# Kernel tuning notes

Hardware: AMD Instinct MI355X
Metric: run time of the kernel (lower is better)

The kernel has to match this reference:

```python
import jax, jax.numpy as jnp
import numpy as np

ROTARY_DIM = 128
ROTARY_BASE = 10000.0
ATTN_SCALE = 11.313708498984761  # sqrt(d_head=128)
N_HEADS = 16
N_KV = 4


def _apply_rotary(x, rotary_dim, rotary_base):
    # x: [seq, heads, d_head]
    seq_len = x.shape[0]
    dim_pairs = rotary_dim // 2
    freqs = 1.0 / rotary_base ** (jnp.arange(dim_pairs, dtype=jnp.float32) / dim_pairs)
    angles = jnp.outer(jnp.arange(seq_len), freqs)  # [seq, pairs]
    cos = jnp.cos(angles)[:, None, :]
    sin = jnp.sin(angles)[:, None, :]
    x_rot = x[..., :rotary_dim]
    x_pass = x[..., rotary_dim:]
    x1 = x_rot[..., ::2]
    x2 = x_rot[..., 1::2]
    out1 = x1 * cos - x2 * sin
    out2 = x1 * sin + x2 * cos
    rotated = jnp.stack([out1, out2], axis=-1).reshape(x_rot.shape)
    return jnp.concatenate([rotated, x_pass], axis=-1)


def setup_inputs() -> dict:
    key = jax.random.key(0)
    ks = jax.random.split(key, 5)
    seq, d_model, d_head = 4096, 2048, 128
    scale = 1.0 / np.sqrt(d_model)
    return {
        "x": jax.random.normal(ks[0], (seq, d_model), jnp.float32),
        "W_Q": jax.random.normal(ks[1], (N_HEADS, d_model, d_head), jnp.float32) * scale,
        "W_K": jax.random.normal(ks[2], (N_KV, d_model, d_head), jnp.float32) * scale,
        "W_V": jax.random.normal(ks[3], (N_KV, d_model, d_head), jnp.float32) * scale,
        "W_O": jax.random.normal(ks[4], (N_HEADS, d_head, d_model), jnp.float32) * scale,
        "b_Q": jnp.zeros((N_HEADS, d_head), jnp.float32),
        "b_K": jnp.zeros((N_KV, d_head), jnp.float32),
        "b_V": jnp.zeros((N_KV, d_head), jnp.float32),
        "b_O": jnp.zeros((2048,), jnp.float32),
    }


def reference(x, W_Q, W_K, W_V, W_O, b_Q, b_K, b_V, b_O):
    seq_len = x.shape[0]
    q = jnp.einsum('sm,nmh->snh', x, W_Q) + b_Q  # [s, 16, 128]
    k = jnp.einsum('sm,nmh->snh', x, W_K) + b_K  # [s, 4, 128]
    v = jnp.einsum('sm,nmh->snh', x, W_V) + b_V
    q = _apply_rotary(q, ROTARY_DIM, ROTARY_BASE)
    k = _apply_rotary(k, ROTARY_DIM, ROTARY_BASE)
    repeats = N_HEADS // N_KV
    k = jnp.repeat(k, repeats, axis=1)
    v = jnp.repeat(v, repeats, axis=1)
    attn_scores = jnp.einsum('qnh,knh->nqk', q, k) / ATTN_SCALE
    mask = jnp.tril(jnp.ones((seq_len, seq_len), dtype=jnp.bool_))
    attn_scores = jnp.where(mask[None, :, :], attn_scores,
                            jnp.finfo(attn_scores.dtype).min)
    pattern = jax.nn.softmax(attn_scores, axis=-1)
    z = jnp.einsum('nqk,knh->qnh', pattern, v)
    return jnp.einsum('snh,nhm->sm', z, W_O) + b_O
```

## Files before the change

### kernel.cpp

```cpp
#include <hip/hip_runtime.h>
#include <hip/hip_bf16.h>
#include <cstdint>
#include <cstddef>

#define SEQ    4096
#define DM     2048
#define DH     128
#define NH     16
#define NKV    4
#define NC     3072
#define KOFF   2048
#define VOFF   2560
#define Q_SCALE 0.12751730f

using bf16 = __hip_bfloat16;
typedef __bf16 bf16x8 __attribute__((ext_vector_type(8)));
typedef float f32x4 __attribute__((ext_vector_type(4)));
typedef float f32x16 __attribute__((ext_vector_type(16)));

static __device__ inline float bf2f(bf16 x) { return __bfloat162float(x); }
static __device__ inline bf16 f2bf(float x) { return __float2bfloat16(x); }

static __device__ inline void load_lds16(const bf16* g, bf16* l) {
    __builtin_amdgcn_global_load_lds(
        (const __attribute__((address_space(1))) uint32_t*)g,
        (__attribute__((address_space(3))) uint32_t*)l, 16, 0, 0);
}

__global__ void xconv(const float* __restrict__ in, bf16* __restrict__ out) {
    int i = blockIdx.x * 256 + threadIdx.x;
    float4 v = ((const float4*)in)[i];
    bf16 a = f2bf(v.x), b = f2bf(v.y), c = f2bf(v.z), d = f2bf(v.w);
    ushort4 u;
    u.x = *(unsigned short*)&a; u.y = *(unsigned short*)&b;
    u.z = *(unsigned short*)&c; u.w = *(unsigned short*)&d;
    ((ushort4*)out)[i] = u;
}

__global__ void prep_wqkv(const float* __restrict__ WQ, const float* __restrict__ WK,
                          const float* __restrict__ WV, bf16* __restrict__ wt) {
    __shared__ float tl[64][65];
    const int t = threadIdx.x;
    const int m0 = (int)blockIdx.x * 64;
    const int head = (int)blockIdx.y >> 1;
    const int h0 = ((int)blockIdx.y & 1) * 64;
    const float* src = (head < 16) ? WQ + (size_t)head * DM * DH
                     : (head < 20) ? WK + (size_t)(head - 16) * DM * DH
                                   : WV + (size_t)(head - 20) * DM * DH;
    {
        const int r = t >> 2, c = (t & 3) * 16;
        const float* p = src + (size_t)(m0 + r) * DH + h0 + c;
        #pragma unroll
        for (int kk = 0; kk < 4; ++kk) {
            float4 v = *(const float4*)(p + kk * 4);
            tl[r][c + kk * 4 + 0] = v.x; tl[r][c + kk * 4 + 1] = v.y;
            tl[r][c + kk * 4 + 2] = v.z; tl[r][c + kk * 4 + 3] = v.w;
        }
    }
    __syncthreads();
    {
        const int hh = t >> 2, ms = (t & 3) * 16;
        const int j = head * 128 + h0 + hh;
        bf16 tmp[16];
        #pragma unroll
        for (int i = 0; i < 16; ++i) tmp[i] = f2bf(tl[ms + i][hh]);
        bf16* q = wt + (size_t)j * DM + m0 + ms;
        *(bf16x8*)q       = *(bf16x8*)&tmp[0];
        *(bf16x8*)(q + 8) = *(bf16x8*)&tmp[8];
    }
}

__global__ void prep_wo(const float* __restrict__ WO, bf16* __restrict__ wt) {
    __shared__ float tl[64][65];
    const int t = threadIdx.x;
    const int m0 = (int)blockIdx.x * 64;
    const int j0 = (int)blockIdx.y * 64;
    {
        const int r = t >> 2, c = (t & 3) * 16;
        const float* p = WO + (size_t)(m0 + r) * DM + j0 + c;
        #pragma unroll
        for (int kk = 0; kk < 4; ++kk) {
            float4 v = *(const float4*)(p + kk * 4);
            tl[r][c + kk * 4 + 0] = v.x; tl[r][c + kk * 4 + 1] = v.y;
            tl[r][c + kk * 4 + 2] = v.z; tl[r][c + kk * 4 + 3] = v.w;
        }
    }
    __syncthreads();
    {
        const int hh = t >> 2, ms = (t & 3) * 16;
        bf16 tmp[16];
        #pragma unroll
        for (int i = 0; i < 16; ++i) tmp[i] = f2bf(tl[ms + i][hh]);
        bf16* q = wt + (size_t)(j0 + hh) * DM + m0 + ms;
        *(bf16x8*)q       = *(bf16x8*)&tmp[0];
        *(bf16x8*)(q + 8) = *(bf16x8*)&tmp[8];
    }
}

__global__ void prep_bias(const float* __restrict__ bQ, const float* __restrict__ bK,
                          const float* __restrict__ bV, float* __restrict__ bias) {
    int j = blockIdx.x * 256 + threadIdx.x;
    if (j >= NC) return;
    bias[j] = (j < KOFF) ? bQ[j] : (j < VOFF ? bK[j - KOFF] : bV[j - VOFF]);
}

__global__ void sctab(float2* __restrict__ tab) {
    int idx = blockIdx.x * 256 + threadIdx.x;
    int s = idx >> 6, i = idx & 63;
    float inv_freq = __expf(-(float)i * 0.14391156831212788f);
    float ang = (float)s * inv_freq;
    float2 cs;
    cs.x = cosf(ang);
    cs.y = sinf(ang);
    tab[idx] = cs;
}

#define BM 128
#define BN 128
#define BK 64

template <typename OutT, int ROT>
__global__ __launch_bounds__(256)
void gemm_bt(const bf16* __restrict__ A, const bf16* __restrict__ Bt,
             const float* __restrict__ bias, OutT* __restrict__ C, int N,
             const float2* __restrict__ tab) {
    __shared__ __align__(16) bf16 As[BM * BK];
    __shared__ __align__(16) bf16 Bs[BN * BK];
    const int tid = threadIdx.x;
    const int wave = tid >> 6, lane = tid & 63;
    const int quad = lane >> 4, l15 = lane & 15;
    const int wm = (wave >> 1) * 64, wn = (wave & 1) * 64;
    const int m0 = blockIdx.y * BM, n0 = blockIdx.x * BN;

    f32x4 acc[4][4] = {};

    const bf16* gsrc = (wave < 2)
        ? A  + (size_t)(m0 + (wave & 1) * 64) * DM
        : Bt + (size_t)(n0 + (wave & 1) * 64) * DM;
    bf16* lbase = (wave < 2 ? As : Bs) + (wave & 1) * 64 * BK;
    const int lrow = lane >> 3;
    const int gslot = (lane & 7) ^ lrow;
    const bf16* gp = gsrc + (size_t)lrow * DM + gslot * 8;

    const int rsw = l15 & 7;

    for (int k0 = 0; k0 < DM; k0 += BK) {
        __syncthreads();
        #pragma unroll
        for (int cc = 0; cc < 8; ++cc)
            load_lds16(gp + (size_t)cc * 8 * DM + k0, lbase + cc * 8 * BK);
        __syncthreads();

        #pragma unroll
        for (int ks = 0; ks < 2; ++ks) {
            bf16x8 af[4], bfr[4];
            #pragma unroll
            for (int i = 0; i < 4; ++i)
                af[i] = *(const bf16x8*)&As[(wm + i * 16 + l15) * BK + (((ks * 4 + quad) ^ rsw) * 8)];
            #pragma unroll
            for (int j = 0; j < 4; ++j)
                bfr[j] = *(const bf16x8*)&Bs[(wn + j * 16 + l15) * BK + (((ks * 4 + quad) ^ rsw) * 8)];
            #pragma unroll
            for (int i = 0; i < 4; ++i)
                #pragma unroll
                for (int j = 0; j < 4; ++j)
                    acc[i][j] = __builtin_amdgcn_mfma_f32_16x16x32_bf16(af[i], bfr[j], acc[i][j], 0, 0, 0);
        }
    }

    const bool doRot = ROT && (n0 < VOFF);
    const float scl = (n0 < KOFF) ? Q_SCALE : 1.0f;

    #pragma unroll
    for (int i = 0; i < 4; ++i) {
        int row = m0 + wm + i * 16 + quad * 4;
        #pragma unroll
        for (int j = 0; j < 4; ++j) {
            int col = n0 + wn + j * 16 + l15;
            float bv = bias[col];
            if (ROT && doRot) {
                const int ii = (col >> 1) & 63;
                const bool odd = col & 1;
                #pragma unroll
                for (int r = 0; r < 4; ++r) {
                    float v = acc[i][j][r] + bv;
                    float pv = __shfl_xor(v, 1);
                    float2 cs = tab[((row + r) << 6) + ii];
                    float o = odd ? (pv * cs.y + v * cs.x) : (v * cs.x - pv * cs.y);
                    C[(size_t)(row + r) * N + col] = (OutT)f2bf(o * scl);
                }
            } else {
                #pragma unroll
                for (int r = 0; r < 4; ++r) {
                    float val = acc[i][j][r] + bv;
                    if constexpr (sizeof(OutT) == 2)
                        C[(size_t)(row + r) * N + col] = f2bf(val);
                    else
                        C[(size_t)(row + r) * N + col] = val;
                }
            }
        }
    }
}

__global__ void vtrans(const bf16* __restrict__ qkv, bf16* __restrict__ vt) {
    __shared__ bf16 tl[64][72];
    const int t = threadIdx.x;
    const int s0 = (int)(blockIdx.x >> 3) * 64;
    const int c0 = (int)(blockIdx.x & 7) * 64;
    {
        int r = t >> 2, cc = (t & 3) * 16;
        const bf16* p = qkv + (size_t)(s0 + r) * NC + VOFF + c0 + cc;
        *(bf16x8*)&tl[r][cc]     = *(const bf16x8*)p;
        *(bf16x8*)&tl[r][cc + 8] = *(const bf16x8*)(p + 8);
    }
    __syncthreads();
    {
        int dd = t >> 2, sc = (t & 3) * 16;
        int col = c0 + dd;
        bf16 tmp[16];
        #pragma unroll
        for (int j = 0; j < 16; ++j) tmp[j] = tl[sc + j][dd];
        bf16* q = vt + (size_t)col * SEQ + s0 + sc;
        *(bf16x8*)q       = *(bf16x8*)&tmp[0];
        *(bf16x8*)(q + 8) = *(bf16x8*)&tmp[8];
    }
}

__global__ __launch_bounds__(256)
void flash(const bf16* __restrict__ qkv, const bf16* __restrict__ vt,
           bf16* __restrict__ z) {
    __shared__ __align__(16) char smem[65536];
    float* ob  = (float*)smem;
    float* lml = (float*)(smem + 32768);

    const int tid = threadIdx.x;
    const int wave = tid >> 6, lane = tid & 63;
    const int l31 = lane & 31, lh = lane >> 5;
    const int ch = wave >> 1;
    const int kh = wave & 1;
    const int bx = blockIdx.x;
    const int qt = 127 - (bx >> 3);
    const int g = (bx >> 1) & 3;
    const int hp = bx & 1;
    const int r_base = qt * 32 + ch * 16;
    const int ktmax = qt >> 1;
    const int rsw = l31 & 7;

    const bf16* kp[4];
    const bf16* vp[4];
    #pragma unroll
    for (int i = 0; i < 4; ++i) {
        const int q = wave * 4 + i;
        const int krow = q * 4 + (lane >> 4);
        kp[i] = qkv + KOFF + g * DH + (size_t)krow * NC + (((lane & 15) ^ (krow & 7)) * 8);
        const int vdd = q * 8 + (lane >> 3);
        vp[i] = vt + (size_t)(g * DH + vdd) * SEQ + (((lane & 7) ^ (vdd & 7)) * 8);
    }

    {
        bf16* Ksb = (bf16*)smem;
        bf16* Vsb = (bf16*)(smem + 16384);
        #pragma unroll
        for (int i = 0; i < 4; ++i) load_lds16(kp[i], Ksb + (wave * 4 + i) * 512);
        #pragma unroll
        for (int i = 0; i < 4; ++i) load_lds16(vp[i], Vsb + (wave * 4 + i) * 512);
        #pragma unroll
        for (int i = 0; i < 4; ++i) { kp[i] += (size_t)64 * NC; vp[i] += 64; }
    }

    bf16x8 qf[8];
    {
        const int qrow = r_base + (l31 & 15);
        const int head = g * 4 + hp * 2 + (l31 >> 4);
        const bf16* qp = qkv + (size_t)qrow * NC + head * DH + lh * 8;
        #pragma unroll
        for (int s = 0; s < 8; ++s)
            qf[s] = *(const bf16x8*)(qp + s * 16);
    }

    f32x16 o_acc[4] = {};
    float lsum = 0.0f;
    int cur = 0;

    for (int kt = 0; kt <= ktmax; ++kt) {
        __syncthreads();
        if (kt < ktmax) {
            bf16* Ksb = (bf16*)(smem + (cur ^ 1) * 32768);
            bf16* Vsb = (bf16*)(smem + (cur ^ 1) * 32768 + 16384);
            #pragma unroll
            for (int i = 0; i < 4; ++i) load_lds16(kp[i], Ksb + (wave * 4 + i) * 512);
            #pragma unroll
            for (int i = 0; i < 4; ++i) load_lds16(vp[i], Vsb + (wave * 4 + i) * 512);
            #pragma unroll
            for (int i = 0; i < 4; ++i) { kp[i] += (size_t)64 * NC; vp[i] += 64; }
        }
        const bf16* Ks = (const bf16*)(smem + cur * 32768);
        const bf16* Vs = (const bf16*)(smem + cur * 32768 + 16384);
        cur ^= 1;

        const int key_min = kt * 64 + kh * 32;
        if (key_min <= r_base + 15) {
            f32x16 sa = {}, sb = {};
            __builtin_amdgcn_s_setprio(1);
            #pragma unroll
            for (int s = 0; s < 4; ++s) {
                bf16x8 kb0 = *(const bf16x8*)&Ks[(kh * 32 + l31) * 128 + (((lh + 4 * s) ^ rsw) * 8)];
                sa = __builtin_amdgcn_mfma_f32_32x32x16_bf16(kb0, qf[2 * s], sa, 0, 0, 0);
                bf16x8 kb1 = *(const bf16x8*)&Ks[(kh * 32 + l31) * 128 + (((lh + 4 * s + 2) ^ rsw) * 8)];
                sb = __builtin_amdgcn_mfma_f32_32x32x16_bf16(kb1, qf[2 * s + 1], sb, 0, 0, 0);
            }
            __builtin_amdgcn_s_setprio(0);
            f32x16 sacc = sa + sb;

            const bool needmask = (key_min + 31 > r_base);
            const int qrow = r_base + (l31 & 15);
            float e[16];
            if (needmask) {
                #pragma unroll
                for (int rg = 0; rg < 16; ++rg) {
                    const int keyg = key_min + (rg & 3) + 8 * (rg >> 2) + 4 * lh;
                    float sv = sacc[rg];
                    if (keyg > qrow) sv = -INFINITY;
                    e[rg] = exp2f(sv);
                }
            } else {
                #pragma unroll
                for (int rg = 0; rg < 16; ++rg)
                    e[rg] = exp2f(sacc[rg]);
            }
            {
                float t0 = (e[0] + e[1]) + (e[2] + e[3]);
                float t1 = (e[4] + e[5]) + (e[6] + e[7]);
                float t2 = (e[8] + e[9]) + (e[10] + e[11]);
                float t3 = (e[12] + e[13]) + (e[14] + e[15]);
                lsum += (t0 + t1) + (t2 + t3);
            }

            bf16x8 pa[2];
            #pragma unroll
            for (int s2 = 0; s2 < 2; ++s2) {
                uint32_t wA0, wA1, wB0, wB1;
                asm("v_cvt_pk_bf16_f32 %0, %1, %2" : "=v"(wA0) : "v"(e[8*s2+0]), "v"(e[8*s2+1]));
                asm("v_cvt_pk_bf16_f32 %0, %1, %2" : "=v"(wA1) : "v"(e[8*s2+2]), "v"(e[8*s2+3]));
                asm("v_cvt_pk_bf16_f32 %0, %1, %2" : "=v"(wB0) : "v"(e[8*s2+4]), "v"(e[8*s2+5]));
                asm("v_cvt_pk_bf16_f32 %0, %1, %2" : "=v"(wB1) : "v"(e[8*s2+6]), "v"(e[8*s2+7]));
                asm volatile("v_permlane32_swap_b32 %0, %1" : "+v"(wA0), "+v"(wB0));
                asm volatile("v_permlane32_swap_b32 %0, %1" : "+v"(wA1), "+v"(wB1));
                union { uint32_t u[4]; bf16x8 v; } cvt;
                cvt.u[0] = wA0; cvt.u[1] = wA1; cvt.u[2] = wB0; cvt.u[3] = wB1;
                pa[s2] = cvt.v;
            }

            __builtin_amdgcn_s_setprio(1);
            #pragma unroll
            for (int s2 = 0; s2 < 2; ++s2) {
                #pragma unroll
                for (int nt = 0; nt < 4; ++nt) {
                    bf16x8 vb = *(const bf16x8*)&Vs[(nt * 32 + l31) * 64 + (((kh * 4 + lh + 2 * s2) ^ rsw) * 8)];
                    o_acc[nt] = __builtin_amdgcn_mfma_f32_32x32x16_bf16(pa[s2], vb, o_acc[nt], 0, 0, 0);
                }
            }
            __builtin_amdgcn_s_setprio(0);
        }
    }

    float la = lsum, lb = lsum;
    asm volatile("v_permlane32_swap_b32 %0, %1" : "+v"(la), "+v"(lb));
    const float l_tot = la + lb;

    __syncthreads();
    if (lh == 0) lml[wave * 32 + l31] = l_tot;
    if (kh == 1) {
        #pragma unroll
        for (int nt = 0; nt < 4; ++nt)
            #pragma unroll
            for (int rg = 0; rg < 16; ++rg) {
                const int m = (rg & 3) + 8 * (rg >> 2) + 4 * lh;
                ob[(ch * 32 + m) * 128 + nt * 32 + l31] = o_acc[nt][rg];
            }
    }
    __syncthreads();
    if (kh == 0) {
        float invl[16];
        #pragma unroll
        for (int rg = 0; rg < 16; ++rg) {
            const int m = (rg & 3) + 8 * (rg >> 2) + 4 * lh;
            invl[rg] = 1.0f / (lml[wave * 32 + m] + lml[(wave + 1) * 32 + m]);
        }
        #pragma unroll
        for (int nt = 0; nt < 4; ++nt)
            #pragma unroll
            for (int rg = 0; rg < 16; ++rg) {
                const int m = (rg & 3) + 8 * (rg >> 2) + 4 * lh;
                float oo = o_acc[nt][rg] + ob[(ch * 32 + m) * 128 + nt * 32 + l31];
                const int row = r_base + (m & 15);
                const int col = (g * 4 + hp * 2 + (m >> 4)) * DH + nt * 32 + l31;
                z[(size_t)row * DM + col] = f2bf(oo * invl[rg]);
            }
    }
}

extern "C" void kernel_launch(void* const* d_in, const int* in_sizes, int n_in,
                              void* d_out, int out_size, void* d_ws, size_t ws_size,
                              hipStream_t stream) {
    const float* x  = (const float*)d_in[0];
    const float* WQ = (const float*)d_in[1];
    const float* WK = (const float*)d_in[2];
    const float* WV = (const float*)d_in[3];
    const float* WO = (const float*)d_in[4];
    const float* bQ = (const float*)d_in[5];
    const float* bK = (const float*)d_in[6];
    const float* bV = (const float*)d_in[7];
    const float* bO = (const float*)d_in[8];
    float* out = (float*)d_out;

    char* ws = (char*)d_ws;
    bf16*  wt_cat = (bf16*)(ws);
    bf16*  wt_o   = (bf16*)(ws + 12582912);
    float* bias_c = (float*)(ws + 20971520);
    bf16*  qkv    = (bf16*)(ws + 20987904);
    bf16*  vt     = (bf16*)(ws + 46153728);
    bf16*  z      = (bf16*)(ws + 50348032);
    bf16*  xb     = (bf16*)(ws + 67125248);
    float2* sct   = (float2*)vt;

    xconv    <<<8192, 256, 0, stream>>>(x, xb);
    prep_wqkv<<<dim3(32, 48), 256, 0, stream>>>(WQ, WK, WV, wt_cat);
    prep_wo  <<<dim3(32, 32), 256, 0, stream>>>(WO, wt_o);
    prep_bias<<<12, 256, 0, stream>>>(bQ, bK, bV, bias_c);
    sctab    <<<1024, 256, 0, stream>>>(sct);
    gemm_bt<bf16, 1> <<<dim3(24, 32), 256, 0, stream>>>(xb, wt_cat, bias_c, qkv, NC, sct);
    vtrans   <<<512, 256, 0, stream>>>(qkv, vt);
    flash    <<<1024, 256, 0, stream>>>(qkv, vt, z);
    gemm_bt<float, 0><<<dim3(16, 32), 256, 0, stream>>>(z, wt_o, bO, out, DM, nullptr);
}
```

Before: 376.5 us.

## Replace double-buffered K/V LDS pipeline with single buffer and serial MFMA chains

```diff
diff --git a/kernel.cpp b/kernel.cpp
--- a/kernel.cpp
+++ b/kernel.cpp
@@ -230,9 +230,11 @@
 __global__ __launch_bounds__(256)
 void flash(const bf16* __restrict__ qkv, const bf16* __restrict__ vt,
            bf16* __restrict__ z) {
-    __shared__ __align__(16) char smem[65536];
+    __shared__ char smem[33280];
+    bf16*  Ks  = (bf16*)smem;
+    bf16*  Vs  = (bf16*)(smem + 16384);
+    float* lml = (float*)(smem + 32768);
     float* ob  = (float*)smem;
-    float* lml = (float*)(smem + 32768);
 
     const int tid = threadIdx.x;
     const int wave = tid >> 6, lane = tid & 63;
@@ -258,17 +260,6 @@
         vp[i] = vt + (size_t)(g * DH + vdd) * SEQ + (((lane & 7) ^ (vdd & 7)) * 8);
     }
 
-    {
-        bf16* Ksb = (bf16*)smem;
-        bf16* Vsb = (bf16*)(smem + 16384);
-        #pragma unroll
-        for (int i = 0; i < 4; ++i) load_lds16(kp[i], Ksb + (wave * 4 + i) * 512);
-        #pragma unroll
-        for (int i = 0; i < 4; ++i) load_lds16(vp[i], Vsb + (wave * 4 + i) * 512);
-        #pragma unroll
-        for (int i = 0; i < 4; ++i) { kp[i] += (size_t)64 * NC; vp[i] += 64; }
-    }
-
     bf16x8 qf[8];
     {
         const int qrow = r_base + (l31 & 15);
@@ -281,37 +272,29 @@
 
     f32x16 o_acc[4] = {};
     float lsum = 0.0f;
-    int cur = 0;
 
     for (int kt = 0; kt <= ktmax; ++kt) {
         __syncthreads();
-        if (kt < ktmax) {
-            bf16* Ksb = (bf16*)(smem + (cur ^ 1) * 32768);
-            bf16* Vsb = (bf16*)(smem + (cur ^ 1) * 32768 + 16384);
-            #pragma unroll
-            for (int i = 0; i < 4; ++i) load_lds16(kp[i], Ksb + (wave * 4 + i) * 512);
-            #pragma unroll
-            for (int i = 0; i < 4; ++i) load_lds16(vp[i], Vsb + (wave * 4 + i) * 512);
-            #pragma unroll
-            for (int i = 0; i < 4; ++i) { kp[i] += (size_t)64 * NC; vp[i] += 64; }
-        }
-        const bf16* Ks = (const bf16*)(smem + cur * 32768);
-        const bf16* Vs = (const bf16*)(smem + cur * 32768 + 16384);
-        cur ^= 1;
+        #pragma unroll
+        for (int i = 0; i < 4; ++i)
+            load_lds16(kp[i], Ks + (wave * 4 + i) * 512);
+        #pragma unroll
+        for (int i = 0; i < 4; ++i)
+            load_lds16(vp[i], Vs + (wave * 4 + i) * 512);
+        __syncthreads();
+        #pragma unroll
+        for (int i = 0; i < 4; ++i) { kp[i] += (size_t)64 * NC; vp[i] += 64; }
 
         const int key_min = kt * 64 + kh * 32;
         if (key_min <= r_base + 15) {
-            f32x16 sa = {}, sb = {};
+            f32x16 sacc = {};
             __builtin_amdgcn_s_setprio(1);
             #pragma unroll
-            for (int s = 0; s < 4; ++s) {
-                bf16x8 kb0 = *(const bf16x8*)&Ks[(kh * 32 + l31) * 128 + (((lh + 4 * s) ^ rsw) * 8)];
-                sa = __builtin_amdgcn_mfma_f32_32x32x16_bf16(kb0, qf[2 * s], sa, 0, 0, 0);
-                bf16x8 kb1 = *(const bf16x8*)&Ks[(kh * 32 + l31) * 128 + (((lh + 4 * s + 2) ^ rsw) * 8)];
-                sb = __builtin_amdgcn_mfma_f32_32x32x16_bf16(kb1, qf[2 * s + 1], sb, 0, 0, 0);
+            for (int s = 0; s < 8; ++s) {
+                bf16x8 kb = *(const bf16x8*)&Ks[(kh * 32 + l31) * 128 + (((lh + 2 * s) ^ rsw) * 8)];
+                sacc = __builtin_amdgcn_mfma_f32_32x32x16_bf16(kb, qf[s], sacc, 0, 0, 0);
             }
             __builtin_amdgcn_s_setprio(0);
-            f32x16 sacc = sa + sb;
 
             const bool needmask = (key_min + 31 > r_base);
             const int qrow = r_base + (l31 & 15);
@@ -354,9 +337,9 @@
 
             __builtin_amdgcn_s_setprio(1);
             #pragma unroll
-            for (int s2 = 0; s2 < 2; ++s2) {
-                #pragma unroll
-                for (int nt = 0; nt < 4; ++nt) {
+            for (int nt = 0; nt < 4; ++nt) {
+                #pragma unroll
+                for (int s2 = 0; s2 < 2; ++s2) {
                     bf16x8 vb = *(const bf16x8*)&Vs[(nt * 32 + l31) * 64 + (((kh * 4 + lh + 2 * s2) ^ rsw) * 8)];
                     o_acc[nt] = __builtin_amdgcn_mfma_f32_32x32x16_bf16(pa[s2], vb, o_acc[nt], 0, 0, 0);
                 }
```

After: 361.5 us. -4.0%, faster.
